# Kernel optimization log

Measured on AMD Instinct MI355X. Metric: run time of the kernel, lower is better.

## Reference

```python
import jax, jax.numpy as jnp
import numpy as np
from jax import lax

STDV = 1.0 / np.sqrt(256.0)  # torch init scale, used to scale random params


def _gru_layer(xs, h0, w_ih, w_hh, b_ih, b_hh):
    # xs: [T, B, I]; h0: [B, H]; w_ih: [3H, I]; w_hh: [3H, H]; biases: [3H]
    H = h0.shape[-1]
    ip = jnp.einsum('tbi,gi->tbg', xs, w_ih) + b_ih  # [T, B, 3H]

    def step(h, ip_t):
        hp = h @ w_hh.T + b_hh  # [B, 3H]
        r = jax.nn.sigmoid(ip_t[:, :H] + hp[:, :H])
        z = jax.nn.sigmoid(ip_t[:, H:2 * H] + hp[:, H:2 * H])
        n = jnp.tanh(ip_t[:, 2 * H:] + r * hp[:, 2 * H:])
        h_new = (1.0 - z) * n + z * h
        return h_new, h_new

    h_last, ys = lax.scan(step, h0, ip)
    return h_last, ys  # [B, H], [T, B, H]


def setup_inputs() -> dict:
    key = jax.random.key(0)
    ks = jax.random.split(key, 7)
    T, B, I, H, L = 2048, 64, 128, 256, 6
    return {
        'x': jax.random.normal(ks[0], (T, B, I), dtype=jnp.float32),
        'h0': jax.random.normal(ks[1], (L, B, H), dtype=jnp.float32),
        'w_ih0': jax.random.normal(ks[2], (3 * H, I), dtype=jnp.float32) * STDV,
        'w_ih_rest': jax.random.normal(ks[3], (L - 1, 3 * H, H), dtype=jnp.float32) * STDV,
        'w_hh': jax.random.normal(ks[4], (L, 3 * H, H), dtype=jnp.float32) * STDV,
        'b_ih': jax.random.normal(ks[5], (L, 3 * H), dtype=jnp.float32) * STDV,
        'b_hh': jax.random.normal(ks[6], (L, 3 * H), dtype=jnp.float32) * STDV,
    }


def reference(x, h0, w_ih0, w_ih_rest, w_hh, b_ih, b_hh):
    num_layers = h0.shape[0]
    h_n = []
    cur = x
    for l in range(num_layers):
        w_ih_l = w_ih0 if l == 0 else w_ih_rest[l - 1]
        h_last, cur = _gru_layer(cur, h0[l], w_ih_l, w_hh[l], b_ih[l], b_hh[l])
        h_n.append(h_last)
    return jnp.stack(h_n)  # [num_layers, B, H]
```

## Files before the change

kernel.cpp:

```cpp
#include <hip/hip_runtime.h>

typedef _Float16 f16;
typedef _Float16 f16x8 __attribute__((ext_vector_type(8)));
typedef _Float16 f16x4 __attribute__((ext_vector_type(4)));
typedef float f32x4 __attribute__((ext_vector_type(4)));

#define T_TOT 2048
#define BATCH 64
#define HID 256
#define G3 768
#define WS 32
#define NWIN 64
#define NRING 4
#define IPT 12288
#define IPSLOT (WS * IPT)

#define NLOG2E -1.44269504088896f
#define P2LOG2E 2.88539008177793f

#define F_YPROG(lg)   (lg)
#define F_IPCONS(lg)  (24 + (lg))
#define F_IPP(lg,q)   (48 + (lg)*4 + (q))
#define F_YC(lg,q)    (144 + (lg)*4 + (q))

__device__ __forceinline__ float fexp2(float x) { return __builtin_amdgcn_exp2f(x); }
__device__ __forceinline__ float frcp(float x) { return __builtin_amdgcn_rcpf(x); }

__device__ __forceinline__ void st_rel(int* p, int v) {
    __hip_atomic_store(p, v, __ATOMIC_RELEASE, __HIP_MEMORY_SCOPE_AGENT);
}
__device__ __forceinline__ int ld_rlx(int* p) {
    return __hip_atomic_load(p, __ATOMIC_RELAXED, __HIP_MEMORY_SCOPE_AGENT);
}
__device__ __forceinline__ void wait_ge(int* f, int target, int tid) {
    if (tid == 0) {
        while (ld_rlx(f) < target) __builtin_amdgcn_s_sleep(4);
        __builtin_amdgcn_fence(__ATOMIC_ACQUIRE, "agent");
    }
    __syncthreads();
}
__device__ __forceinline__ void wait4_ge(int* f, int target, int tid) {
    if (tid == 0) {
        #pragma unroll
        for (int q = 0; q < 4; ++q)
            while (ld_rlx(f + q) < target) __builtin_amdgcn_s_sleep(4);
        __builtin_amdgcn_fence(__ATOMIC_ACQUIRE, "agent");
    }
    __syncthreads();
}
__device__ __forceinline__ void bar_lgkm() {
    asm volatile("s_waitcnt lgkmcnt(0)\n\ts_barrier" ::: "memory");
}

__global__ void cvt_f16(const float* __restrict__ s, f16* __restrict__ d, int n) {
    int i = (blockIdx.x * 256 + threadIdx.x) * 4;
    if (i + 3 < n) {
        f32x4 v = *(const f32x4*)(s + i);
        f16x4 o = { (f16)v[0], (f16)v[1], (f16)v[2], (f16)v[3] };
        *(f16x4*)(d + i) = o;
    }
}

__global__ void cvt_whh(const float* __restrict__ s, f16* __restrict__ d, int n) {
    int i = (blockIdx.x * 256 + threadIdx.x) * 4;
    if (i + 3 < n) {
        int row = (i >> 8) % G3;
        float sc = (row < 512) ? NLOG2E : P2LOG2E;
        f32x4 v = *(const f32x4*)(s + i);
        f16x4 o = { (f16)(v[0] * sc), (f16)(v[1] * sc), (f16)(v[2] * sc), (f16)(v[3] * sc) };
        *(f16x4*)(d + i) = o;
    }
}

__global__ void bias_prep(const float* __restrict__ bi, const float* __restrict__ bh,
                          float* __restrict__ o) {
    int i = blockIdx.x * 256 + threadIdx.x;
    if (i < 6 * G3) {
        int g = i % G3;
        float sc = (g < 512) ? NLOG2E : P2LOG2E;
        o[i] = sc * (bi[i] + (g < 512 ? bh[i] : 0.0f));
    }
}

__global__ void bhn_prep(const float* __restrict__ bh, float* __restrict__ o) {
    int l = blockIdx.x, j = threadIdx.x;
    o[l * 256 + j] = P2LOG2E * bh[l * G3 + 512 + j];
}

__device__ void scan_role(const f16* __restrict__ ipring, f16* __restrict__ yring,
                          const f16* __restrict__ whh, const float* __restrict__ bhns,
                          const float* __restrict__ h0, float* __restrict__ out,
                          int* flags, char* smem, int l, int g, int tid) {
    f16* hb = (f16*)smem;
    const int wv = tid >> 6, lane = tid & 63;
    const int quad = lane >> 4, b = lane & 15;
    const int gbase = 32 * wv + quad * 4;
    const int lg = l * 4 + g;
    const int kk0 = 4 * wv + (quad >> 1);
    const int wsub = (quad & 1) * 4;

    f16x8 wf[6][8];
    #pragma unroll
    for (int i = 0; i < 6; ++i) {
        const f16* wp = whh + (long)l * G3 * HID
                      + ((i >> 1) * 256 + 32 * wv + (i & 1) * 16 + b) * 256 + quad * 8;
        #pragma unroll
        for (int kf = 0; kf < 8; ++kf)
            wf[i][kf] = *(const f16x8*)(wp + kf * 32);
    }
    f32x4 bhn[2];
    bhn[0] = *(const f32x4*)(bhns + l * 256 + gbase);
    bhn[1] = *(const f32x4*)(bhns + l * 256 + gbase + 16);

    {
        int k = tid >> 4, bb = tid & 15;
        const float* hp = h0 + (long)(l * 64 + g * 16 + bb) * HID + k * 8;
        f32x4 v0 = *(const f32x4*)hp;
        f32x4 v1 = *(const f32x4*)(hp + 4);
        f16x8 h8 = { (f16)v0[0], (f16)v0[1], (f16)v0[2], (f16)v0[3],
                     (f16)v1[0], (f16)v1[1], (f16)v1[2], (f16)v1[3] };
        *(f16x8*)(&hb[(k * 16 + bb) * 8]) = h8;
    }
    f16x4 hp_[2];
    #pragma unroll
    for (int s = 0; s < 2; ++s) {
        f32x4 v = *(const f32x4*)(h0 + (long)(l * 64 + g * 16 + b) * HID + gbase + s * 16);
        hp_[s] = (f16x4){ (f16)v[0], (f16)v[1], (f16)v[2], (f16)v[3] };
    }
    __syncthreads();

    const int lane_off = (wv * 4 + quad) * 128 + b * 8;
    for (int w = 0; w < NWIN; ++w) {
        if (l < 5 && w >= NRING)
            wait4_ge(flags + F_YC(lg, 0), w - NRING + 1, tid);
        wait4_ge(flags + F_IPP(lg, 0), w + 1, tid);
        const int slot = w & (NRING - 1);
        const f16* ipt = ipring + (long)(lg * NRING + slot) * IPSLOT + lane_off;
        f16* yc = yring + (((long)lg * NRING + slot) * 512 + b) * HID + gbase;
        f16x8 p0 = *(const f16x8*)(ipt);
        f16x8 p1 = *(const f16x8*)(ipt + 4096);
        f16x8 p2 = *(const f16x8*)(ipt + 8192);
        for (int tp = 0; tp < WS; tp += 2) {
            #pragma unroll
            for (int u = 0; u < 2; ++u) {
                const int rdo = u * 4096;
                const int wro = (u ^ 1) * 4096;
                f32x4 acc[6];
                acc[0] = acc[1] = acc[2] = acc[3] = (f32x4){0.f, 0.f, 0.f, 0.f};
                acc[4] = bhn[0];
                acc[5] = bhn[1];
                #pragma unroll
                for (int kf = 0; kf < 8; ++kf) {
                    f16x8 hf = *(const f16x8*)(&hb[rdo + ((kf * 4 + quad) * 16 + b) * 8]);
                    #pragma unroll
                    for (int i = 0; i < 6; ++i)
                        acc[i] = __builtin_amdgcn_mfma_f32_16x16x32_f16(
                            wf[i][kf], hf, acc[i], 0, 0, 0);
                }
                f16x4 hnew[2];
                #pragma unroll
                for (int s = 0; s < 2; ++s) {
                    #pragma unroll
                    for (int r = 0; r < 4; ++r) {
                        float rr = frcp(1.0f + fexp2(acc[s][r] + (float)p0[s * 4 + r]));
                        float zz = frcp(1.0f + fexp2(acc[2 + s][r] + (float)p1[s * 4 + r]));
                        float tt = frcp(1.0f + fexp2((float)p2[s * 4 + r] + rr * acc[4 + s][r]));
                        float nn = 1.0f - 2.0f * tt;
                        hnew[s][r] = (f16)(nn + zz * ((float)hp_[s][r] - nn));
                    }
                    hp_[s] = hnew[s];
                    *(f16x4*)(&hb[wro + ((kk0 + 2 * s) * 16 + b) * 8 + wsub]) = hnew[s];
                }
                if (tp + u + 1 < WS) ipt += IPT;
                p0 = *(const f16x8*)(ipt);
                p1 = *(const f16x8*)(ipt + 4096);
                p2 = *(const f16x8*)(ipt + 8192);
                if (l < 5) {
                    *(f16x4*)(yc) = hnew[0];
                    *(f16x4*)(yc + 16) = hnew[1];
                }
                yc += 16 * HID;
                bar_lgkm();
            }
        }
        __syncthreads();
        if (tid == 0) {
            st_rel(flags + F_IPCONS(lg), w + 1);
            if (l < 5) st_rel(flags + F_YPROG(lg), w + 1);
        }
    }
    {
        int k = tid >> 4, bb = tid & 15;
        f16x8 h8 = *(const f16x8*)(&hb[(k * 16 + bb) * 8]);
        float* op = out + (long)(l * 64 + g * 16 + bb) * HID + k * 8;
        f32x4 v0 = { (float)h8[0], (float)h8[1], (float)h8[2], (float)h8[3] };
        f32x4 v1 = { (float)h8[4], (float)h8[5], (float)h8[6], (float)h8[7] };
        *(f32x4*)op = v0;
        *(f32x4*)(op + 4) = v1;
    }
}

template<int K>
__device__ void worker_role(const f16* __restrict__ src, bool is_x, int g,
                            const f16* __restrict__ Wl, const float* __restrict__ bias,
                            f16* __restrict__ dstb, int* flags,
                            int lay, int lg, int plg, int q,
                            char* smem, int tid) {
    f16* As = (f16*)smem;
    const int wv = tid >> 6, lane = tid & 63;
    const int quad = lane >> 4, l16 = lane & 15;
    const int mi = wv & 3, ni = wv >> 2;
    constexpr int CPR = K / 8;

    for (int w = 0; w < NWIN; ++w) {
        if (lay > 0) wait_ge(flags + F_YPROG(plg), w + 1, tid);
        if (w >= NRING) wait_ge(flags + F_IPCONS(lg), w - NRING + 1, tid);
        const int slot = w & (NRING - 1);
        f16* dst = dstb + (long)slot * IPSLOT;
        #pragma unroll
        for (int it = 0; it < (128 * CPR) / 512; ++it) {
            int idx = it * 512 + tid;
            int row = idx / CPR, c8 = idx % CPR;
            int wr = q * 128 + row;
            long soff;
            if (is_x) soff = ((long)(w * WS + (wr >> 4)) * 64 + g * 16 + (wr & 15)) * K + c8 * 8;
            else      soff = ((long)slot * 512 + wr) * K + c8 * 8;
            f16x8 v = *(const f16x8*)(src + soff);
            *(f16x8*)(&As[row * K + (c8 ^ (row & 7)) * 8]) = v;
        }
        __syncthreads();
        for (int nt = 0; nt < 6; ++nt) {
            const int cbase = nt * 128 + ni * 64;
            f16x8 bc[4], bn[4];
            #pragma unroll
            for (int ns = 0; ns < 4; ++ns)
                bc[ns] = *(const f16x8*)(Wl + (long)(cbase + ns * 16 + l16) * K + quad * 8);
            f32x4 acc[2][4];
            #pragma unroll
            for (int i = 0; i < 2; ++i)
                #pragma unroll
                for (int j = 0; j < 4; ++j) acc[i][j] = (f32x4){0.f, 0.f, 0.f, 0.f};
            #pragma unroll
            for (int kf = 0; kf < K / 32; ++kf) {
                if (kf + 1 < K / 32) {
                    #pragma unroll
                    for (int ns = 0; ns < 4; ++ns)
                        bn[ns] = *(const f16x8*)(Wl + (long)(cbase + ns * 16 + l16) * K
                                                 + (kf + 1) * 32 + quad * 8);
                }
                f16x8 af[2];
                #pragma unroll
                for (int ms = 0; ms < 2; ++ms) {
                    int row = 32 * mi + 16 * ms + l16;
                    int c8 = (kf * 4 + quad) ^ (row & 7);
                    af[ms] = *(const f16x8*)(&As[row * K + c8 * 8]);
                }
                #pragma unroll
                for (int ms = 0; ms < 2; ++ms)
                    #pragma unroll
                    for (int ns = 0; ns < 4; ++ns)
                        acc[ms][ns] = __builtin_amdgcn_mfma_f32_16x16x32_f16(
                            af[ms], bc[ns], acc[ms][ns], 0, 0, 0);
                #pragma unroll
                for (int ns = 0; ns < 4; ++ns) bc[ns] = bn[ns];
            }
            #pragma unroll
            for (int ns = 0; ns < 4; ++ns) {
                int col = cbase + ns * 16 + l16;
                float bv = bias[col];
                float sc = (col < 512) ? NLOG2E : P2LOG2E;
                int gate = col >> 8, j = col & 255;
                int wv2 = j >> 5, rem = j & 31;
                int s2 = rem >> 4, q2 = (rem & 15) >> 2, r2 = rem & 3;
                #pragma unroll
                for (int ms = 0; ms < 2; ++ms) {
                    int t2 = q * 8 + 2 * mi + ms;
                    f16* dp = dst + t2 * IPT + ((gate * 8 + wv2) * 4 + q2) * 128
                            + s2 * 4 + r2;
                    #pragma unroll
                    for (int r = 0; r < 4; ++r)
                        dp[(quad * 4 + r) * 8] = (f16)(acc[ms][ns][r] * sc + bv);
                }
            }
        }
        __syncthreads();
        if (tid == 0) {
            st_rel(flags + F_IPP(lg, q), w + 1);
            if (lay > 0) st_rel(flags + F_YC(plg, q), w + 1);
        }
    }
}

__global__ __launch_bounds__(512, 2) void gru_fused(
        const f16* __restrict__ xh, const f16* __restrict__ wih,
        const f16* __restrict__ whh, const float* __restrict__ biasc,
        const float* __restrict__ bhns, const float* __restrict__ h0,
        float* __restrict__ out, f16* __restrict__ yring, f16* __restrict__ ipring,
        int* flags) {
    __shared__ __align__(16) char smem[65536];
    const int bid = blockIdx.x, tid = threadIdx.x;
    const int x = bid & 7, j = bid >> 3;
    const int lgrp = j / 5, role = j % 5;
    const int lg = lgrp * 8 + x;
    const int l = lg >> 2, g = lg & 3;
    if (role == 0) {
        scan_role(ipring, yring, whh, bhns, h0, out, flags, smem, l, g, tid);
    } else {
        const int q = role - 1;
        const float* bias = biasc + l * G3;
        f16* dstb = ipring + (long)lg * NRING * IPSLOT;
        if (l == 0) {
            worker_role<128>(xh, true, g, wih, bias, dstb, flags,
                             0, lg, 0, q, smem, tid);
        } else {
            int plg = (l - 1) * 4 + g;
            const f16* Wl = wih + 768 * 128 + (long)(l - 1) * G3 * HID;
            const f16* src = yring + (long)plg * NRING * 512 * HID;
            worker_role<256>(src, false, g, Wl, bias, dstb, flags,
                             l, lg, plg, q, smem, tid);
        }
    }
}

extern "C" void kernel_launch(void* const* d_in, const int* in_sizes, int n_in,
                              void* d_out, int out_size, void* d_ws, size_t ws_size,
                              hipStream_t stream) {
    const float* x     = (const float*)d_in[0];
    const float* h0    = (const float*)d_in[1];
    const float* w_ih0 = (const float*)d_in[2];
    const float* w_ihr = (const float*)d_in[3];
    const float* w_hh  = (const float*)d_in[4];
    const float* b_ih  = (const float*)d_in[5];
    const float* b_hh  = (const float*)d_in[6];
    float* out = (float*)d_out;

    char* p = (char*)d_ws;
    f16* xh      = (f16*)p;   p += (long)T_TOT * BATCH * 128 * 2;
    f16* wih     = (f16*)p;   p += (long)(768 * 128 + 5 * 768 * 256) * 2;
    f16* whh     = (f16*)p;   p += (long)6 * 768 * 256 * 2;
    float* biasc = (float*)p; p += (long)6 * G3 * 4;
    float* bhns  = (float*)p; p += (long)6 * 256 * 4;
    f16* yring   = (f16*)p;   p += (long)20 * NRING * 512 * HID * 2;
    f16* ipring  = (f16*)p;   p += (long)24 * NRING * IPSLOT * 2;
    int* flags   = (int*)p;   p += 1024;

    hipMemsetAsync(flags, 0, 1024, stream);
    cvt_f16<<<16384, 256, 0, stream>>>(x, xh, T_TOT * BATCH * 128);
    cvt_f16<<<96, 256, 0, stream>>>(w_ih0, wih, 768 * 128);
    cvt_f16<<<960, 256, 0, stream>>>(w_ihr, wih + 768 * 128, 5 * 768 * 256);
    cvt_whh<<<1152, 256, 0, stream>>>(w_hh, whh, 6 * 768 * 256);
    bias_prep<<<18, 256, 0, stream>>>(b_ih, b_hh, biasc);
    bhn_prep<<<6, 256, 0, stream>>>(b_hh, bhns);

    gru_fused<<<120, 512, 0, stream>>>(xh, wih, whh, biasc, bhns, h0, out,
                                       yring, ipring, flags);
}
```

Baseline: 5.194 ms.

## Double block size to split GRU recurrence gate work across sixteen waves

Launches the fused GRU kernel with 1024 threads per block. Each scan wave now computes 16 hidden dims for all three gates, so it runs 24 MFMAs per timestep instead of 48, which shortens the serial per-step critical path. The input-projection roles are remapped to use the extra waves, with fewer column tiles per wave and wider staging loads. It also adds a spin budget to the flag waits so a stalled wait eventually exits, which risks silently wrong results instead of a hang. The larger block means more waves meeting at each per-step barrier and higher register pressure under a 1024-thread launch bound.

```diff
diff --git a/kernel.cpp b/kernel.cpp
--- a/kernel.cpp
+++ b/kernel.cpp
@@ -18,6 +18,8 @@
 #define NLOG2E -1.44269504088896f
 #define P2LOG2E 2.88539008177793f
 
+#define SPIN_BUDGET 20000000L
+
 #define F_YPROG(lg)   (lg)
 #define F_IPCONS(lg)  (24 + (lg))
 #define F_IPP(lg,q)   (48 + (lg)*4 + (q))
@@ -32,18 +34,24 @@
 __device__ __forceinline__ int ld_rlx(int* p) {
     return __hip_atomic_load(p, __ATOMIC_RELAXED, __HIP_MEMORY_SCOPE_AGENT);
 }
-__device__ __forceinline__ void wait_ge(int* f, int target, int tid) {
+__device__ __forceinline__ void wait_ge(int* f, int target, int tid, long& budget) {
     if (tid == 0) {
-        while (ld_rlx(f) < target) __builtin_amdgcn_s_sleep(4);
+        while (ld_rlx(f) < target) {
+            if (--budget < 0) break;
+            __builtin_amdgcn_s_sleep(4);
+        }
         __builtin_amdgcn_fence(__ATOMIC_ACQUIRE, "agent");
     }
     __syncthreads();
 }
-__device__ __forceinline__ void wait4_ge(int* f, int target, int tid) {
+__device__ __forceinline__ void wait4_ge(int* f, int target, int tid, long& budget) {
     if (tid == 0) {
         #pragma unroll
         for (int q = 0; q < 4; ++q)
-            while (ld_rlx(f + q) < target) __builtin_amdgcn_s_sleep(4);
+            while (ld_rlx(f + q) < target) {
+                if (--budget < 0) break;
+                __builtin_amdgcn_s_sleep(4);
+            }
         __builtin_amdgcn_fence(__ATOMIC_ACQUIRE, "agent");
     }
     __syncthreads();
@@ -94,49 +102,49 @@
     f16* hb = (f16*)smem;
     const int wv = tid >> 6, lane = tid & 63;
     const int quad = lane >> 4, b = lane & 15;
-    const int gbase = 32 * wv + quad * 4;
+    const int dbase = 16 * wv;
     const int lg = l * 4 + g;
-    const int kk0 = 4 * wv + (quad >> 1);
-    const int wsub = (quad & 1) * 4;
-
-    f16x8 wf[6][8];
+    long budget = SPIN_BUDGET;
+
+    f16x8 wf[3][8];
     #pragma unroll
-    for (int i = 0; i < 6; ++i) {
+    for (int gate = 0; gate < 3; ++gate) {
         const f16* wp = whh + (long)l * G3 * HID
-                      + ((i >> 1) * 256 + 32 * wv + (i & 1) * 16 + b) * 256 + quad * 8;
+                      + (gate * 256 + dbase + b) * 256 + quad * 8;
         #pragma unroll
         for (int kf = 0; kf < 8; ++kf)
-            wf[i][kf] = *(const f16x8*)(wp + kf * 32);
-    }
-    f32x4 bhn[2];
-    bhn[0] = *(const f32x4*)(bhns + l * 256 + gbase);
-    bhn[1] = *(const f32x4*)(bhns + l * 256 + gbase + 16);
-
-    {
-        int k = tid >> 4, bb = tid & 15;
-        const float* hp = h0 + (long)(l * 64 + g * 16 + bb) * HID + k * 8;
+            wf[gate][kf] = *(const f16x8*)(wp + kf * 32);
+    }
+    f32x4 bhn = *(const f32x4*)(bhns + l * 256 + dbase + 4 * quad);
+
+    if (tid < 512) {
+        int kgrp = tid >> 4, bb = tid & 15;
+        const float* hp = h0 + (long)(l * 64 + g * 16 + bb) * HID + kgrp * 8;
         f32x4 v0 = *(const f32x4*)hp;
         f32x4 v1 = *(const f32x4*)(hp + 4);
         f16x8 h8 = { (f16)v0[0], (f16)v0[1], (f16)v0[2], (f16)v0[3],
                      (f16)v1[0], (f16)v1[1], (f16)v1[2], (f16)v1[3] };
-        *(f16x8*)(&hb[(k * 16 + bb) * 8]) = h8;
-    }
-    f16x4 hp_[2];
-    #pragma unroll
-    for (int s = 0; s < 2; ++s) {
-        f32x4 v = *(const f32x4*)(h0 + (long)(l * 64 + g * 16 + b) * HID + gbase + s * 16);
-        hp_[s] = (f16x4){ (f16)v[0], (f16)v[1], (f16)v[2], (f16)v[3] };
+        *(f16x8*)(&hb[(kgrp * 16 + bb) * 8]) = h8;
+    }
+    f16x4 hp_;
+    {
+        f32x4 v = *(const f32x4*)(h0 + (long)(l * 64 + g * 16 + b) * HID + dbase + 4 * quad);
+        hp_ = (f16x4){ (f16)v[0], (f16)v[1], (f16)v[2], (f16)v[3] };
     }
     __syncthreads();
 
-    const int lane_off = (wv * 4 + quad) * 128 + b * 8;
+    const int lane_off = ((wv >> 1) * 4 + quad) * 128 + b * 8;
+    const int sub = 4 * (wv & 1);
+    const int hwoff = ((2 * wv + (quad >> 1)) * 16 + b) * 8 + 4 * (quad & 1);
+    const int dimc = dbase + 4 * quad;
+
     for (int w = 0; w < NWIN; ++w) {
         if (l < 5 && w >= NRING)
-            wait4_ge(flags + F_YC(lg, 0), w - NRING + 1, tid);
-        wait4_ge(flags + F_IPP(lg, 0), w + 1, tid);
+            wait4_ge(flags + F_YC(lg, 0), w - NRING + 1, tid, budget);
+        wait4_ge(flags + F_IPP(lg, 0), w + 1, tid, budget);
         const int slot = w & (NRING - 1);
-        const f16* ipt = ipring + (long)(lg * NRING + slot) * IPSLOT + lane_off;
-        f16* yc = yring + (((long)lg * NRING + slot) * 512 + b) * HID + gbase;
+        const f16* ipt = ipring + ((long)lg * NRING + slot) * IPSLOT + lane_off;
+        f16* yc = yring + (((long)lg * NRING + slot) * 512 + b) * HID + dimc;
         f16x8 p0 = *(const f16x8*)(ipt);
         f16x8 p1 = *(const f16x8*)(ipt + 4096);
         f16x8 p2 = *(const f16x8*)(ipt + 8192);
@@ -145,40 +153,35 @@
             for (int u = 0; u < 2; ++u) {
                 const int rdo = u * 4096;
                 const int wro = (u ^ 1) * 4096;
-                f32x4 acc[6];
-                acc[0] = acc[1] = acc[2] = acc[3] = (f32x4){0.f, 0.f, 0.f, 0.f};
-                acc[4] = bhn[0];
-                acc[5] = bhn[1];
-                #pragma unroll
-                for (int kf = 0; kf < 8; ++kf) {
-                    f16x8 hf = *(const f16x8*)(&hb[rdo + ((kf * 4 + quad) * 16 + b) * 8]);
-                    #pragma unroll
-                    for (int i = 0; i < 6; ++i)
-                        acc[i] = __builtin_amdgcn_mfma_f32_16x16x32_f16(
-                            wf[i][kf], hf, acc[i], 0, 0, 0);
-                }
-                f16x4 hnew[2];
-                #pragma unroll
-                for (int s = 0; s < 2; ++s) {
-                    #pragma unroll
-                    for (int r = 0; r < 4; ++r) {
-                        float rr = frcp(1.0f + fexp2(acc[s][r] + (float)p0[s * 4 + r]));
-                        float zz = frcp(1.0f + fexp2(acc[2 + s][r] + (float)p1[s * 4 + r]));
-                        float tt = frcp(1.0f + fexp2((float)p2[s * 4 + r] + rr * acc[4 + s][r]));
-                        float nn = 1.0f - 2.0f * tt;
-                        hnew[s][r] = (f16)(nn + zz * ((float)hp_[s][r] - nn));
-                    }
-                    hp_[s] = hnew[s];
-                    *(f16x4*)(&hb[wro + ((kk0 + 2 * s) * 16 + b) * 8 + wsub]) = hnew[s];
-                }
+                f16x8 hf[8];
+                #pragma unroll
+                for (int kk = 0; kk < 8; ++kk)
+                    hf[kk] = *(const f16x8*)(&hb[rdo + ((kk * 4 + quad) * 16 + b) * 8]);
+                f32x4 acc0 = (f32x4){0.f, 0.f, 0.f, 0.f};
+                f32x4 acc1 = (f32x4){0.f, 0.f, 0.f, 0.f};
+                f32x4 acc2 = bhn;
+                #pragma unroll
+                for (int kk = 0; kk < 8; ++kk) {
+                    acc0 = __builtin_amdgcn_mfma_f32_16x16x32_f16(wf[0][kk], hf[kk], acc0, 0, 0, 0);
+                    acc1 = __builtin_amdgcn_mfma_f32_16x16x32_f16(wf[1][kk], hf[kk], acc1, 0, 0, 0);
+                    acc2 = __builtin_amdgcn_mfma_f32_16x16x32_f16(wf[2][kk], hf[kk], acc2, 0, 0, 0);
+                }
+                f16x4 hnew;
+                #pragma unroll
+                for (int r = 0; r < 4; ++r) {
+                    float rr = frcp(1.0f + fexp2(acc0[r] + (float)p0[sub + r]));
+                    float zz = frcp(1.0f + fexp2(acc1[r] + (float)p1[sub + r]));
+                    float tt = frcp(1.0f + fexp2((float)p2[sub + r] + rr * acc2[r]));
+                    float nn = 1.0f - 2.0f * tt;
+                    hnew[r] = (f16)(nn + zz * ((float)hp_[r] - nn));
+                }
+                hp_ = hnew;
+                *(f16x4*)(&hb[wro + hwoff]) = hnew;
                 if (tp + u + 1 < WS) ipt += IPT;
                 p0 = *(const f16x8*)(ipt);
                 p1 = *(const f16x8*)(ipt + 4096);
                 p2 = *(const f16x8*)(ipt + 8192);
-                if (l < 5) {
-                    *(f16x4*)(yc) = hnew[0];
-                    *(f16x4*)(yc + 16) = hnew[1];
-                }
+                if (l < 5) *(f16x4*)(yc) = hnew;
                 yc += 16 * HID;
                 bar_lgkm();
             }
@@ -190,13 +193,15 @@
         }
     }
     {
-        int k = tid >> 4, bb = tid & 15;
-        f16x8 h8 = *(const f16x8*)(&hb[(k * 16 + bb) * 8]);
-        float* op = out + (long)(l * 64 + g * 16 + bb) * HID + k * 8;
-        f32x4 v0 = { (float)h8[0], (float)h8[1], (float)h8[2], (float)h8[3] };
-        f32x4 v1 = { (float)h8[4], (float)h8[5], (float)h8[6], (float)h8[7] };
-        *(f32x4*)op = v0;
-        *(f32x4*)(op + 4) = v1;
+        if (tid < 512) {
+            int kgrp = tid >> 4, bb = tid & 15;
+            f16x8 h8 = *(const f16x8*)(&hb[(kgrp * 16 + bb) * 8]);
+            float* op = out + (long)(l * 64 + g * 16 + bb) * HID + kgrp * 8;
+            f32x4 v0 = { (float)h8[0], (float)h8[1], (float)h8[2], (float)h8[3] };
+            f32x4 v1 = { (float)h8[4], (float)h8[5], (float)h8[6], (float)h8[7] };
+            *(f32x4*)op = v0;
+            *(f32x4*)(op + 4) = v1;
+        }
     }
 }
 
@@ -211,15 +216,16 @@
     const int quad = lane >> 4, l16 = lane & 15;
     const int mi = wv & 3, ni = wv >> 2;
     constexpr int CPR = K / 8;
+    long budget = SPIN_BUDGET;
 
     for (int w = 0; w < NWIN; ++w) {
-        if (lay > 0) wait_ge(flags + F_YPROG(plg), w + 1, tid);
-        if (w >= NRING) wait_ge(flags + F_IPCONS(lg), w - NRING + 1, tid);
+        if (lay > 0) wait_ge(flags + F_YPROG(plg), w + 1, tid, budget);
+        if (w >= NRING) wait_ge(flags + F_IPCONS(lg), w - NRING + 1, tid, budget);
         const int slot = w & (NRING - 1);
         f16* dst = dstb + (long)slot * IPSLOT;
         #pragma unroll
-        for (int it = 0; it < (128 * CPR) / 512; ++it) {
-            int idx = it * 512 + tid;
+        for (int it = 0; it < (128 * CPR) / 1024; ++it) {
+            int idx = it * 1024 + tid;
             int row = idx / CPR, c8 = idx % CPR;
             int wr = q * 128 + row;
             long soff;
@@ -229,8 +235,8 @@
             *(f16x8*)(&As[row * K + (c8 ^ (row & 7)) * 8]) = v;
         }
         __syncthreads();
-        for (int nt = 0; nt < 6; ++nt) {
-            const int cbase = nt * 128 + ni * 64;
+        for (int nt = 0; nt < 3; ++nt) {
+            const int cbase = nt * 256 + ni * 64;
             f16x8 bc[4], bn[4];
             #pragma unroll
             for (int ns = 0; ns < 4; ++ns)
@@ -291,7 +297,7 @@
     }
 }
 
-__global__ __launch_bounds__(512, 2) void gru_fused(
+__global__ __launch_bounds__(1024, 1) void gru_fused(
         const f16* __restrict__ xh, const f16* __restrict__ wih,
         const f16* __restrict__ whh, const float* __restrict__ biasc,
         const float* __restrict__ bhns, const float* __restrict__ h0,
@@ -352,6 +358,6 @@
     bias_prep<<<18, 256, 0, stream>>>(b_ih, b_hh, biasc);
     bhn_prep<<<6, 256, 0, stream>>>(b_hh, bhns);
 
-    gru_fused<<<120, 512, 0, stream>>>(xh, wih, whh, biasc, bhns, h0, out,
-                                       yring, ipring, flags);
-}
+    gru_fused<<<120, 1024, 0, stream>>>(xh, wih, whh, biasc, bhns, h0, out,
+                                        yring, ipring, flags);
+}
```

New measurement: 9.942 ms. +91.4%, slower.
